# Kernel optimization log

Hardware: AMD Instinct MI355X
Metric: run time of the kernel (lower is better)

The kernel has to match this reference:

```python
import jax, jax.numpy as jnp
import numpy as np

H = 16  # n_heads

def _rmsnorm(x, g, eps=1e-6):
    return x * jax.lax.rsqrt(jnp.mean(x * x, axis=-1, keepdims=True) + eps) * g

def _rope_diag(L, hd, dtype):
    # Diagonal of the full [L, hd, hd] rotary matrix: cos(pos * theta_pair) at every dim.
    # (The torch einsum 'bhld,ldd->bhld' extracts this diagonal, so no pairwise rotation occurs.)
    pair = jnp.arange(hd) // 2
    theta = 10000.0 ** (-2.0 * pair / hd)
    return jnp.cos(jnp.arange(L)[:, None].astype(jnp.float32) * theta[None, :]).astype(dtype)


def setup_inputs() -> dict:
    key = jax.random.key(0)
    ks = jax.random.split(key, 8)
    B, L, E = 2, 2048, 2048
    F = 2 * E  # SwiGLU width
    s = 0.02
    return {
        "x": jax.random.normal(ks[0], (B, L, E), jnp.float32),
        "g": jnp.ones((E,), jnp.float32),
        "wq": jax.random.normal(ks[1], (E, E), jnp.float32) * s,
        "wk": jax.random.normal(ks[2], (E, E), jnp.float32) * s,
        "wv": jax.random.normal(ks[3], (E, E), jnp.float32) * s,
        "w1": jax.random.normal(ks[4], (E, F), jnp.float32) * s,
        "b1": jnp.zeros((F,), jnp.float32),
        "wg": jax.random.normal(ks[5], (F, F), jnp.float32) * s,
        "bg": jnp.zeros((F,), jnp.float32),
        "wl": jax.random.normal(ks[6], (F, F), jnp.float32) * s,
        "bl": jnp.zeros((F,), jnp.float32),
        "beta": jnp.ones((1,), jnp.float32),
        "w2": jax.random.normal(ks[7], (F, E), jnp.float32) * s,
        "b2": jnp.zeros((E,), jnp.float32),
    }


def reference(x, g, wq, wk, wv, w1, b1, wg, bg, wl, bl, beta, w2, b2):
    B, L, E = x.shape
    hd = E // H
    x_res = x
    h = _rmsnorm(x, g)
    # projections -> [B, H, L, hd]
    q = (h @ wq).reshape(B, L, H, hd).transpose(0, 2, 1, 3)
    k = (h @ wk).reshape(B, L, H, hd).transpose(0, 2, 1, 3)
    v = (h @ wv).reshape(B, L, H, hd).transpose(0, 2, 1, 3)
    D = _rope_diag(L, hd, x.dtype)  # [L, hd], diagonal of rotary matrix
    q = q * D
    k = k * D
    score = jnp.einsum('bhld,bhmd->bhlm', q, k)  # [B,H,L,L]
    # causal mask added BEFORE scaling (faithful to source)
    mask = jnp.triu(jnp.full((L, L), -jnp.inf, dtype=score.dtype), k=1)
    score = (score + mask) / jnp.sqrt(jnp.asarray(hd, score.dtype))
    attn = jax.nn.softmax(score, axis=-1)
    o = jnp.einsum('bhlm,bhmd->bhld', attn, v)
    o = o.transpose(0, 2, 1, 3).reshape(B, L, E)
    x = o + x_res
    x_res = x
    h = _rmsnorm(x, g)
    h = h @ w1 + b1  # [B, L, 2E]
    gate = h @ wg + bg
    lin = h @ wl + bl
    act = gate * jax.nn.sigmoid(beta * gate) * lin
    out = act @ w2 + b2
    return out + x_res
```

## Files before the change

### kernel.cpp

```cpp
#include <hip/hip_runtime.h>
#include <cstdint>
#include <math.h>


typedef _Float16 f16;
typedef _Float16 f16x8 __attribute__((ext_vector_type(8)));
typedef _Float16 f16x4 __attribute__((ext_vector_type(4)));
typedef float    f32x4 __attribute__((ext_vector_type(4)));

#define MFMA_16x16x32(a, b, c) __builtin_amdgcn_mfma_f32_16x16x32_f16(a, b, c, 0, 0, 0)

__device__ __forceinline__ void gload_lds16(const void* g, void* lds) {
  __builtin_amdgcn_global_load_lds(
      (__attribute__((address_space(1))) void*)(uintptr_t)g,
      (__attribute__((address_space(3))) void*)(unsigned)(uintptr_t)lds,
      16, 0, 0);
}

__global__ void convT_k(const float* __restrict__ W, f16* __restrict__ Wt,
                        int K, int N) {
  __shared__ float tile[32][33];
  const int n0 = blockIdx.x << 5, k0 = blockIdx.y << 5;
  const int t = threadIdx.x;
  const int r = t >> 3, c4 = (t & 7) << 2;
  const f32x4 v = *(const f32x4*)(W + (size_t)(k0 + r) * N + n0 + c4);
  tile[r][c4 + 0] = v[0]; tile[r][c4 + 1] = v[1];
  tile[r][c4 + 2] = v[2]; tile[r][c4 + 3] = v[3];
  __syncthreads();
  f16x4 o;
  o[0] = (f16)tile[c4 + 0][r]; o[1] = (f16)tile[c4 + 1][r];
  o[2] = (f16)tile[c4 + 2][r]; o[3] = (f16)tile[c4 + 3][r];
  *(f16x4*)(Wt + (size_t)(n0 + r) * K + k0 + c4) = o;
}

__global__ void rope_tab_k(float* __restrict__ Dt) {
  const int l = blockIdx.x, d = threadIdx.x;
  const float th = __expf(-0.0719557841f * (float)(d & ~1));
  Dt[(l << 7) + d] = cosf((float)l * th);
}

__global__ void rmsnorm_k(const float* __restrict__ X, const float* __restrict__ G,
                          f16* __restrict__ H) {
  __shared__ float red[4];
  const int row = blockIdx.x, t = threadIdx.x;
  const float* xp = X + ((size_t)row << 11) + (t << 3);
  const f32x4 v0 = *(const f32x4*)xp;
  const f32x4 v1 = *(const f32x4*)(xp + 4);
  float ss = v0[0]*v0[0] + v0[1]*v0[1] + v0[2]*v0[2] + v0[3]*v0[3]
           + v1[0]*v1[0] + v1[1]*v1[1] + v1[2]*v1[2] + v1[3]*v1[3];
#pragma unroll
  for (int m = 1; m < 64; m <<= 1) ss += __shfl_xor(ss, m);
  if ((t & 63) == 0) red[t >> 6] = ss;
  __syncthreads();
  const float tot = red[0] + red[1] + red[2] + red[3];
  const float rs = rsqrtf(tot * (1.f / 2048.f) + 1e-6f);
  const float* gp = G + (t << 3);
  const f32x4 g0 = *(const f32x4*)gp, g1 = *(const f32x4*)(gp + 4);
  f16x8 o;
  o[0] = (f16)(v0[0]*rs*g0[0]); o[1] = (f16)(v0[1]*rs*g0[1]);
  o[2] = (f16)(v0[2]*rs*g0[2]); o[3] = (f16)(v0[3]*rs*g0[3]);
  o[4] = (f16)(v1[0]*rs*g1[0]); o[5] = (f16)(v1[1]*rs*g1[1]);
  o[6] = (f16)(v1[2]*rs*g1[2]); o[7] = (f16)(v1[3]*rs*g1[3]);
  *(f16x8*)(H + ((size_t)row << 11) + (t << 3)) = o;
}

__global__ void vtrans_k(const f16* __restrict__ V, f16* __restrict__ Vt) {
  __shared__ f16 tile[32][36];
  const int l0 = blockIdx.x << 5, d0 = blockIdx.y << 5, bh = blockIdx.z;
  const int b = bh >> 4, h = bh & 15;
  const int t = threadIdx.x;
  const int r = t >> 3, c4 = (t & 7) << 2;
  const f16x4 v = *(const f16x4*)(V + (size_t)((b << 11) + l0 + r) * 2048 + (h << 7) + d0 + c4);
  tile[r][c4 + 0] = v[0]; tile[r][c4 + 1] = v[1];
  tile[r][c4 + 2] = v[2]; tile[r][c4 + 3] = v[3];
  __syncthreads();
  f16x4 o;
  o[0] = tile[c4 + 0][r]; o[1] = tile[c4 + 1][r];
  o[2] = tile[c4 + 2][r]; o[3] = tile[c4 + 3][r];
  *(f16x4*)(Vt + (size_t)((bh << 7) + d0 + r) * 2048 + l0 + c4) = o;
}

template <int EPI>
__launch_bounds__(256, 2)
__global__ void gemm_k(const f16* __restrict__ A, const f16* __restrict__ Bt,
                       void* __restrict__ Cout, int M, int N, int K,
                       const float* __restrict__ bias,
                       const float* __restrict__ auxf,
                       const f16* __restrict__ auxh,
                       const float* __restrict__ betap,
                       float scale) {
  __shared__ alignas(16) f16 As[128 * 64];
  __shared__ alignas(16) f16 Bs[128 * 64];
  const int t = threadIdx.x;
  const int lane = t & 63;
  const int w = t >> 6;
  const int wm = w >> 1, wn = w & 1;
  const int bm = blockIdx.y << 7;
  const int bn = blockIdx.x << 7;
  const int lh = lane & 15, lq = lane >> 4;

  f32x4 acc[4][4] = {};

  for (int k0 = 0; k0 < K; k0 += 64) {
    __syncthreads();
#pragma unroll
    for (int i = 0; i < 4; ++i) {
      const int idx = i * 256 + (w << 6) + lane;
      const int row = idx >> 3, c = idx & 7;
      const int cs = (c ^ (row & 7)) << 3;
      gload_lds16(A + (size_t)(bm + row) * K + k0 + cs,
                  &As[(i * 256 + (w << 6)) << 3]);
      gload_lds16(Bt + (size_t)(bn + row) * K + k0 + cs,
                  &Bs[(i * 256 + (w << 6)) << 3]);
    }
    asm volatile("s_waitcnt vmcnt(0)" ::: "memory");
    __syncthreads();
#pragma unroll
    for (int kk = 0; kk < 2; ++kk) {
      f16x8 af[4], bf[4];
#pragma unroll
      for (int mi = 0; mi < 4; ++mi) {
        const int r = (wm << 6) + (mi << 4) + lh;
        af[mi] = *(const f16x8*)&As[(r << 6) + ((((kk << 2) + lq) ^ (r & 7)) << 3)];
      }
#pragma unroll
      for (int ni = 0; ni < 4; ++ni) {
        const int r = (wn << 6) + (ni << 4) + lh;
        bf[ni] = *(const f16x8*)&Bs[(r << 6) + ((((kk << 2) + lq) ^ (r & 7)) << 3)];
      }
#pragma unroll
      for (int mi = 0; mi < 4; ++mi)
#pragma unroll
        for (int ni = 0; ni < 4; ++ni)
          acc[mi][ni] = MFMA_16x16x32(af[mi], bf[ni], acc[mi][ni]);
    }
  }

  const float be = (EPI == 3) ? betap[0] : 0.f;
#pragma unroll
  for (int mi = 0; mi < 4; ++mi) {
#pragma unroll
    for (int ni = 0; ni < 4; ++ni) {
#pragma unroll
      for (int r = 0; r < 4; ++r) {
        const int grow = bm + (wm << 6) + (mi << 4) + (lq << 2) + r;
        const int gcol = bn + (wn << 6) + (ni << 4) + lh;
        float v = acc[mi][ni][r];
        if (EPI >= 2) v += bias[gcol];
        const size_t off = (size_t)grow * N + gcol;
        if (EPI == 0) {
          v *= scale * auxf[((grow & 2047) << 7) + (gcol & 127)];
          ((f16*)Cout)[off] = (f16)v;
        } else if (EPI == 1 || EPI == 2) {
          ((f16*)Cout)[off] = (f16)v;
        } else if (EPI == 3) {
          ((f16*)Cout)[off] = (f16)(v / (1.f + __expf(-be * v)));
        } else if (EPI == 4) {
          ((f16*)Cout)[off] = (f16)(v * (float)auxh[off]);
        } else {
          ((float*)Cout)[off] = v + auxf[off];
        }
      }
    }
  }
}

__launch_bounds__(256, 2)
__global__ void attn_k(const f16* __restrict__ Q, const f16* __restrict__ Kb,
                       const f16* __restrict__ Vt, const float* __restrict__ Xres,
                       float* __restrict__ X2) {
  constexpr int L = 2048, E = 2048, HD = 128;
  __shared__ alignas(16) f16 Ks[64 * 128];
  __shared__ alignas(16) f16 Vs[128 * 64];
  __shared__ alignas(16) f16 Ps[4][32 * 72];

  const int t = threadIdx.x, lane = t & 63, w = t >> 6;
  const int q0 = blockIdx.x << 7;
  const int bh = blockIdx.y;
  const int b = bh >> 4, h = bh & 15;
  const int lh = lane & 15, lq = lane >> 4;
  const int wrow0 = q0 + (w << 5);

  f16x8 qf[2][4];
#pragma unroll
  for (int mi = 0; mi < 2; ++mi) {
    const f16* qrow = Q + (size_t)(b * L + wrow0 + (mi << 4) + lh) * E + h * HD;
#pragma unroll
    for (int kq = 0; kq < 4; ++kq)
      qf[mi][kq] = *(const f16x8*)(qrow + (kq << 5) + (lq << 3));
  }

  f32x4 oacc[2][8] = {};
  float mrun[2][4], lrun[2][4];
#pragma unroll
  for (int mi = 0; mi < 2; ++mi)
#pragma unroll
    for (int r = 0; r < 4; ++r) { mrun[mi][r] = -1e30f; lrun[mi][r] = 0.f; }

  const int nkv = q0 + 128;
  for (int kv0 = 0; kv0 < nkv; kv0 += 64) {
    __syncthreads();
#pragma unroll
    for (int i = 0; i < 4; ++i) {
      const int idx = i * 256 + (w << 6) + lane;
      {
        const int row = idx >> 4, c = idx & 15;
        gload_lds16(Kb + (size_t)(b * L + kv0 + row) * E + h * HD + ((c ^ (row & 7)) << 3),
                    &Ks[(i * 256 + (w << 6)) << 3]);
      }
      {
        const int row = idx >> 3, c = idx & 7;
        gload_lds16(Vt + ((size_t)bh * HD + row) * L + kv0 + ((c ^ (row & 7)) << 3),
                    &Vs[(i * 256 + (w << 6)) << 3]);
      }
    }
    asm volatile("s_waitcnt vmcnt(0)" ::: "memory");
    __syncthreads();

    if (kv0 <= wrow0 + 31) {
      f32x4 sacc[2][4] = {};
#pragma unroll
      for (int kq = 0; kq < 4; ++kq) {
        f16x8 kf[4];
#pragma unroll
        for (int ni = 0; ni < 4; ++ni) {
          const int r = (ni << 4) + lh;
          kf[ni] = *(const f16x8*)&Ks[(r << 7) + ((((kq << 2) + lq) ^ (r & 7)) << 3)];
        }
#pragma unroll
        for (int mi = 0; mi < 2; ++mi)
#pragma unroll
          for (int ni = 0; ni < 4; ++ni)
            sacc[mi][ni] = MFMA_16x16x32(qf[mi][kq], kf[ni], sacc[mi][ni]);
      }
      if (kv0 + 63 > wrow0) {
#pragma unroll
        for (int mi = 0; mi < 2; ++mi)
#pragma unroll
          for (int ni = 0; ni < 4; ++ni)
#pragma unroll
            for (int r = 0; r < 4; ++r) {
              const int qr = wrow0 + (mi << 4) + (lq << 2) + r;
              const int kv = kv0 + (ni << 4) + lh;
              if (kv > qr) sacc[mi][ni][r] = -1e30f;
            }
      }
      float scl[2][4], rsum[2][4];
#pragma unroll
      for (int mi = 0; mi < 2; ++mi)
#pragma unroll
        for (int r = 0; r < 4; ++r) {
          float v = fmaxf(fmaxf(sacc[mi][0][r], sacc[mi][1][r]),
                          fmaxf(sacc[mi][2][r], sacc[mi][3][r]));
          v = fmaxf(v, __shfl_xor(v, 1));
          v = fmaxf(v, __shfl_xor(v, 2));
          v = fmaxf(v, __shfl_xor(v, 4));
          v = fmaxf(v, __shfl_xor(v, 8));
          const float mnew = fmaxf(mrun[mi][r], v);
          scl[mi][r] = __expf(mrun[mi][r] - mnew);
          mrun[mi][r] = mnew;
          rsum[mi][r] = 0.f;
        }
#pragma unroll
      for (int mi = 0; mi < 2; ++mi)
#pragma unroll
        for (int ni = 0; ni < 4; ++ni)
#pragma unroll
          for (int r = 0; r < 4; ++r) {
            const float p = __expf(sacc[mi][ni][r] - mrun[mi][r]);
            rsum[mi][r] += p;
            Ps[w][((mi << 4) + (lq << 2) + r) * 72 + (ni << 4) + lh] = (f16)p;
          }
#pragma unroll
      for (int mi = 0; mi < 2; ++mi)
#pragma unroll
        for (int r = 0; r < 4; ++r) {
          float s = rsum[mi][r];
          s += __shfl_xor(s, 1);
          s += __shfl_xor(s, 2);
          s += __shfl_xor(s, 4);
          s += __shfl_xor(s, 8);
          lrun[mi][r] = lrun[mi][r] * scl[mi][r] + s;
        }
#pragma unroll
      for (int mi = 0; mi < 2; ++mi)
#pragma unroll
        for (int nd = 0; nd < 8; ++nd)
#pragma unroll
          for (int r = 0; r < 4; ++r) oacc[mi][nd][r] *= scl[mi][r];
#pragma unroll
      for (int kp = 0; kp < 2; ++kp) {
        f16x8 pf[2];
#pragma unroll
        for (int mi = 0; mi < 2; ++mi)
          pf[mi] = *(const f16x8*)&Ps[w][((mi << 4) + lh) * 72 + (kp << 5) + (lq << 3)];
#pragma unroll
        for (int nd = 0; nd < 8; ++nd) {
          const int r = (nd << 4) + lh;
          const f16x8 vf = *(const f16x8*)&Vs[(r << 6) + ((((kp << 2) + lq) ^ (r & 7)) << 3)];
#pragma unroll
          for (int mi = 0; mi < 2; ++mi)
            oacc[mi][nd] = MFMA_16x16x32(pf[mi], vf, oacc[mi][nd]);
        }
      }
    }
  }
#pragma unroll
  for (int mi = 0; mi < 2; ++mi)
#pragma unroll
    for (int nd = 0; nd < 8; ++nd)
#pragma unroll
      for (int r = 0; r < 4; ++r) {
        const int qr = wrow0 + (mi << 4) + (lq << 2) + r;
        const size_t off = (size_t)(b * L + qr) * E + h * HD + (nd << 4) + lh;
        X2[off] = oacc[mi][nd][r] / lrun[mi][r] + Xres[off];
      }
}

extern "C" void kernel_launch(void* const* d_in, const int* in_sizes, int n_in,
                              void* d_out, int out_size, void* d_ws, size_t ws_size,
                              hipStream_t stream) {
  const float* x    = (const float*)d_in[0];
  const float* g    = (const float*)d_in[1];
  const float* wq   = (const float*)d_in[2];
  const float* wk   = (const float*)d_in[3];
  const float* wv   = (const float*)d_in[4];
  const float* w1   = (const float*)d_in[5];
  const float* b1   = (const float*)d_in[6];
  const float* wgp  = (const float*)d_in[7];
  const float* bg   = (const float*)d_in[8];
  const float* wl   = (const float*)d_in[9];
  const float* bl   = (const float*)d_in[10];
  const float* beta = (const float*)d_in[11];
  const float* w2   = (const float*)d_in[12];
  const float* b2   = (const float*)d_in[13];

  constexpr size_t MB = 1ull << 20;
  char* ws = (char*)d_ws;
  f16*   wT   = (f16*)(ws + 0 * MB);
  float* Dt   = (float*)(ws + 32 * MB);
  f16*   hbuf = (f16*)(ws + 33 * MB);
  f16*   qbuf = (f16*)(ws + 49 * MB);
  f16*   kbuf = (f16*)(ws + 65 * MB);
  f16*   vbuf = (f16*)(ws + 81 * MB);
  f16*   vtb  = (f16*)(ws + 97 * MB);
  float* x2   = (float*)(ws + 113 * MB);
  f16*   a1   = (f16*)(ws + 49 * MB);
  f16*   sbuf = (f16*)(ws + 81 * MB);
  f16*   act  = (f16*)(ws + 145 * MB);
  (void)ws_size; (void)n_in; (void)in_sizes; (void)out_size;

  const dim3 blk(256);
  const float qscale = 0.08838834764831845f;

  rope_tab_k<<<2048, 128, 0, stream>>>(Dt);
  rmsnorm_k<<<4096, blk, 0, stream>>>(x, g, hbuf);

  convT_k<<<dim3(64, 64), blk, 0, stream>>>(wq, wT, 2048, 2048);
  gemm_k<0><<<dim3(16, 32), blk, 0, stream>>>(hbuf, wT, qbuf, 4096, 2048, 2048,
                                              nullptr, Dt, nullptr, nullptr, qscale);
  convT_k<<<dim3(64, 64), blk, 0, stream>>>(wk, wT, 2048, 2048);
  gemm_k<0><<<dim3(16, 32), blk, 0, stream>>>(hbuf, wT, kbuf, 4096, 2048, 2048,
                                              nullptr, Dt, nullptr, nullptr, 1.0f);
  convT_k<<<dim3(64, 64), blk, 0, stream>>>(wv, wT, 2048, 2048);
  gemm_k<1><<<dim3(16, 32), blk, 0, stream>>>(hbuf, wT, vbuf, 4096, 2048, 2048,
                                              nullptr, nullptr, nullptr, nullptr, 1.0f);
  vtrans_k<<<dim3(64, 4, 32), blk, 0, stream>>>(vbuf, vtb);

  attn_k<<<dim3(16, 32), blk, 0, stream>>>(qbuf, kbuf, vtb, x, x2);

  rmsnorm_k<<<4096, blk, 0, stream>>>(x2, g, hbuf);

  convT_k<<<dim3(128, 64), blk, 0, stream>>>(w1, wT, 2048, 4096);
  gemm_k<2><<<dim3(32, 32), blk, 0, stream>>>(hbuf, wT, a1, 4096, 4096, 2048,
                                              b1, nullptr, nullptr, nullptr, 1.0f);
  convT_k<<<dim3(128, 128), blk, 0, stream>>>(wgp, wT, 4096, 4096);
  gemm_k<3><<<dim3(32, 32), blk, 0, stream>>>(a1, wT, sbuf, 4096, 4096, 4096,
                                              bg, nullptr, nullptr, beta, 1.0f);
  convT_k<<<dim3(128, 128), blk, 0, stream>>>(wl, wT, 4096, 4096);
  gemm_k<4><<<dim3(32, 32), blk, 0, stream>>>(a1, wT, act, 4096, 4096, 4096,
                                              bl, nullptr, sbuf, nullptr, 1.0f);
  convT_k<<<dim3(64, 128), blk, 0, stream>>>(w2, wT, 4096, 2048);
  gemm_k<5><<<dim3(16, 32), blk, 0, stream>>>(act, wT, (float*)d_out, 4096, 2048, 4096,
                                              b2, x2, nullptr, nullptr, 1.0f);
}
```

Baseline: 765.5 us.

## Add pipelined 256x256 GEMM, fuse QKV projection, persistent causal attention scheduling

Introduces a 512-thread GEMM with 256x256 tiles and double-buffered LDS, plus interleaved prefetch and priority hints, for the QKV and FFN projections. The three Q/K/V projections become one GEMM over a concatenated transposed weight, with per-segment rope and scale applied in the epilogue. Attention becomes a persistent kernel that pulls work items from an atomic counter, taking the longest causal query blocks first to balance load. Costs include higher LDS and register use per block, and a memset plus atomic per block.

```diff
diff --git a/kernel.cpp b/kernel.cpp
--- a/kernel.cpp
+++ b/kernel.cpp
@@ -81,14 +81,145 @@
 }
 
 template <int EPI>
+__launch_bounds__(512, 2)
+__global__ void gemm256_k(const f16* __restrict__ A, const f16* __restrict__ Bt,
+                          void* __restrict__ Cout, int M, int N, int K,
+                          const float* __restrict__ bias,
+                          const float* __restrict__ auxf,
+                          const f16* __restrict__ auxh,
+                          const float* __restrict__ betap, float scale) {
+  __shared__ alignas(16) f16 lds[65536];
+  const int t = threadIdx.x, lane = t & 63, w = t >> 6;
+  const int wm = w >> 2, wn = w & 3;
+  const int bm = blockIdx.y << 8, bn = blockIdx.x << 8;
+  const int lh = lane & 15, lq = lane >> 4;
+  const int NT = K >> 6;
+  const int lrow = lane >> 3;
+  const int lco  = ((lane & 7) ^ lrow) << 3;
+
+  const f16* Agl = A  + (size_t)(bm + lrow) * K + lco;
+  const f16* Bgl = Bt + (size_t)(bn + lrow) * K + lco;
+  const int aw = w << 3;
+  const int bw = w << 4;
+
+  f32x4 acc[8][4] = {};
+  f16x8 bf[4][2];
+
+  auto stA = [&](int tile, int half) {
+    const int d = (tile & 1) << 15;
+    const int k0 = tile << 6;
+    const int r0 = aw + (half << 6);
+    gload_lds16(Agl + (size_t)r0 * K + k0, (void*)&lds[d + r0 * 64]);
+    gload_lds16(Agl + (size_t)(r0 + 128) * K + k0, (void*)&lds[d + (r0 + 128) * 64]);
+  };
+  auto stB = [&](int tile, int half) {
+    const int d = ((tile & 1) << 15) + 16384;
+    const int k0 = tile << 6;
+    const int r0 = bw + (half << 7);
+    gload_lds16(Bgl + (size_t)r0 * K + k0, (void*)&lds[d + r0 * 64]);
+    gload_lds16(Bgl + (size_t)(r0 + 8) * K + k0, (void*)&lds[d + (r0 + 8) * 64]);
+  };
+  auto ldA = [&](int d, int mi, int kk) {
+    const int r = (wm << 7) + (mi << 4) + lh;
+    return *(const f16x8*)&lds[(d << 15) + r * 64 + ((((kk << 2) + lq) ^ (lh & 7)) << 3)];
+  };
+  auto ldB = [&](int d, int ni, int kk) {
+    const int r = (wn << 6) + (ni << 4) + lh;
+    return *(const f16x8*)&lds[(d << 15) + 16384 + r * 64 + ((((kk << 2) + lq) ^ (lh & 7)) << 3)];
+  };
+
+  stB(0, 0); stB(0, 1); stA(0, 0); stA(0, 1);
+  stB(1, 0); stB(1, 1); stA(1, 0);
+  asm volatile("s_waitcnt vmcnt(6)" ::: "memory");
+  __builtin_amdgcn_s_barrier();
+
+  for (int tt = 0; tt < NT; tt += 2) {
+    const bool pf = (tt + 2 < NT);
+#pragma unroll
+    for (int hf = 0; hf < 2; ++hf) {
+#pragma unroll
+      for (int ph = 0; ph < 4; ++ph) {
+        f16x8 a0k0 = ldA(hf, 2 * ph, 0),     a0k1 = ldA(hf, 2 * ph, 1);
+        f16x8 a1k0 = ldA(hf, 2 * ph + 1, 0), a1k1 = ldA(hf, 2 * ph + 1, 1);
+        if (ph == 0) {
+#pragma unroll
+          for (int ni = 0; ni < 4; ++ni) {
+            bf[ni][0] = ldB(hf, ni, 0); bf[ni][1] = ldB(hf, ni, 1);
+          }
+        }
+        if (hf == 0) {
+          if (ph == 0) stA(tt + 1, 1);
+          else if (ph == 1) { if (pf) stB(tt + 2, 0); }
+          else if (ph == 2) { if (pf) stB(tt + 2, 1); }
+          else              { if (pf) stA(tt + 2, 0); }
+        } else {
+          if (ph == 0)      { if (pf) stA(tt + 2, 1); }
+          else if (ph == 1) { if (pf) stB(tt + 3, 0); }
+          else if (ph == 2) { if (pf) stB(tt + 3, 1); }
+          else              { if (pf) stA(tt + 3, 0); }
+        }
+        __builtin_amdgcn_s_barrier();
+        __builtin_amdgcn_sched_barrier(0);
+        __builtin_amdgcn_s_setprio(1);
+#pragma unroll
+        for (int ni = 0; ni < 4; ++ni) {
+          acc[2 * ph][ni]     = MFMA_16x16x32(a0k0, bf[ni][0], acc[2 * ph][ni]);
+          acc[2 * ph][ni]     = MFMA_16x16x32(a0k1, bf[ni][1], acc[2 * ph][ni]);
+          acc[2 * ph + 1][ni] = MFMA_16x16x32(a1k0, bf[ni][0], acc[2 * ph + 1][ni]);
+          acc[2 * ph + 1][ni] = MFMA_16x16x32(a1k1, bf[ni][1], acc[2 * ph + 1][ni]);
+        }
+        __builtin_amdgcn_s_setprio(0);
+        __builtin_amdgcn_sched_barrier(0);
+        if (ph == 3) {
+          if (hf == 0) {
+            if (pf) asm volatile("s_waitcnt vmcnt(6)" ::: "memory");
+            else    asm volatile("s_waitcnt vmcnt(0)" ::: "memory");
+          } else if (pf) {
+            asm volatile("s_waitcnt vmcnt(6)" ::: "memory");
+          }
+        }
+        __builtin_amdgcn_s_barrier();
+      }
+    }
+  }
+
+  const float be = (EPI == 3) ? betap[0] : 0.f;
+#pragma unroll
+  for (int mi = 0; mi < 8; ++mi) {
+#pragma unroll
+    for (int ni = 0; ni < 4; ++ni) {
+#pragma unroll
+      for (int r = 0; r < 4; ++r) {
+        const int grow = bm + (wm << 7) + (mi << 4) + (lq << 2) + r;
+        const int gcol = bn + (wn << 6) + (ni << 4) + lh;
+        float v = acc[mi][ni][r];
+        if (EPI >= 2 && EPI <= 4) v += bias[gcol];
+        if (EPI == 6) {
+          const int seg = gcol >> 11, c = gcol & 2047;
+          if (seg < 2) {
+            const float f = auxf[((grow & 2047) << 7) + (c & 127)];
+            v *= (seg == 0) ? scale * f : f;
+          }
+          ((f16*)Cout)[(size_t)seg * 8388608 + ((size_t)grow << 11) + c] = (f16)v;
+        } else if (EPI == 2) {
+          ((f16*)Cout)[(size_t)grow * N + gcol] = (f16)v;
+        } else if (EPI == 3) {
+          ((f16*)Cout)[(size_t)grow * N + gcol] = (f16)(v / (1.f + __expf(-be * v)));
+        } else if (EPI == 4) {
+          const size_t off = (size_t)grow * N + gcol;
+          ((f16*)Cout)[off] = (f16)(v * (float)auxh[off]);
+        }
+      }
+    }
+  }
+}
+
+template <int EPI>
 __launch_bounds__(256, 2)
 __global__ void gemm_k(const f16* __restrict__ A, const f16* __restrict__ Bt,
                        void* __restrict__ Cout, int M, int N, int K,
                        const float* __restrict__ bias,
-                       const float* __restrict__ auxf,
-                       const f16* __restrict__ auxh,
-                       const float* __restrict__ betap,
-                       float scale) {
+                       const float* __restrict__ auxf) {
   __shared__ alignas(16) f16 As[128 * 64];
   __shared__ alignas(16) f16 Bs[128 * 64];
   const int t = threadIdx.x;
@@ -117,7 +248,7 @@
     __syncthreads();
 #pragma unroll
     for (int kk = 0; kk < 2; ++kk) {
-      f16x8 af[4], bf[4];
+      f16x8 af[4], bfr[4];
 #pragma unroll
       for (int mi = 0; mi < 4; ++mi) {
         const int r = (wm << 6) + (mi << 4) + lh;
@@ -126,17 +257,16 @@
 #pragma unroll
       for (int ni = 0; ni < 4; ++ni) {
         const int r = (wn << 6) + (ni << 4) + lh;
-        bf[ni] = *(const f16x8*)&Bs[(r << 6) + ((((kk << 2) + lq) ^ (r & 7)) << 3)];
+        bfr[ni] = *(const f16x8*)&Bs[(r << 6) + ((((kk << 2) + lq) ^ (r & 7)) << 3)];
       }
 #pragma unroll
       for (int mi = 0; mi < 4; ++mi)
 #pragma unroll
         for (int ni = 0; ni < 4; ++ni)
-          acc[mi][ni] = MFMA_16x16x32(af[mi], bf[ni], acc[mi][ni]);
+          acc[mi][ni] = MFMA_16x16x32(af[mi], bfr[ni], acc[mi][ni]);
     }
   }
 
-  const float be = (EPI == 3) ? betap[0] : 0.f;
 #pragma unroll
   for (int mi = 0; mi < 4; ++mi) {
 #pragma unroll
@@ -145,21 +275,9 @@
       for (int r = 0; r < 4; ++r) {
         const int grow = bm + (wm << 6) + (mi << 4) + (lq << 2) + r;
         const int gcol = bn + (wn << 6) + (ni << 4) + lh;
-        float v = acc[mi][ni][r];
-        if (EPI >= 2) v += bias[gcol];
+        float v = acc[mi][ni][r] + bias[gcol];
         const size_t off = (size_t)grow * N + gcol;
-        if (EPI == 0) {
-          v *= scale * auxf[((grow & 2047) << 7) + (gcol & 127)];
-          ((f16*)Cout)[off] = (f16)v;
-        } else if (EPI == 1 || EPI == 2) {
-          ((f16*)Cout)[off] = (f16)v;
-        } else if (EPI == 3) {
-          ((f16*)Cout)[off] = (f16)(v / (1.f + __expf(-be * v)));
-        } else if (EPI == 4) {
-          ((f16*)Cout)[off] = (f16)(v * (float)auxh[off]);
-        } else {
-          ((float*)Cout)[off] = v + auxf[off];
-        }
+        ((float*)Cout)[off] = v + auxf[off];
       }
     }
   }
@@ -168,153 +286,161 @@
 __launch_bounds__(256, 2)
 __global__ void attn_k(const f16* __restrict__ Q, const f16* __restrict__ Kb,
                        const f16* __restrict__ Vt, const float* __restrict__ Xres,
-                       float* __restrict__ X2) {
+                       float* __restrict__ X2, int* __restrict__ qcnt) {
   constexpr int L = 2048, E = 2048, HD = 128;
   __shared__ alignas(16) f16 Ks[64 * 128];
   __shared__ alignas(16) f16 Vs[128 * 64];
   __shared__ alignas(16) f16 Ps[4][32 * 72];
+  __shared__ int s_item;
 
   const int t = threadIdx.x, lane = t & 63, w = t >> 6;
-  const int q0 = blockIdx.x << 7;
-  const int bh = blockIdx.y;
-  const int b = bh >> 4, h = bh & 15;
   const int lh = lane & 15, lq = lane >> 4;
-  const int wrow0 = q0 + (w << 5);
-
-  f16x8 qf[2][4];
-#pragma unroll
-  for (int mi = 0; mi < 2; ++mi) {
-    const f16* qrow = Q + (size_t)(b * L + wrow0 + (mi << 4) + lh) * E + h * HD;
-#pragma unroll
-    for (int kq = 0; kq < 4; ++kq)
-      qf[mi][kq] = *(const f16x8*)(qrow + (kq << 5) + (lq << 3));
+
+  for (;;) {
+    if (t == 0) s_item = atomicAdd(qcnt, 1);
+    __syncthreads();
+    const int item = s_item;
+    if (item >= 512) return;
+    const int bh = item & 31;
+    const int q0 = (15 - (item >> 5)) << 7;
+    const int b = bh >> 4, h = bh & 15;
+    const int wrow0 = q0 + (w << 5);
+
+    f16x8 qf[2][4];
+#pragma unroll
+    for (int mi = 0; mi < 2; ++mi) {
+      const f16* qrow = Q + (size_t)(b * L + wrow0 + (mi << 4) + lh) * E + h * HD;
+#pragma unroll
+      for (int kq = 0; kq < 4; ++kq)
+        qf[mi][kq] = *(const f16x8*)(qrow + (kq << 5) + (lq << 3));
+    }
+
+    f32x4 oacc[2][8] = {};
+    float mrun[2][4], lrun[2][4];
+#pragma unroll
+    for (int mi = 0; mi < 2; ++mi)
+#pragma unroll
+      for (int r = 0; r < 4; ++r) { mrun[mi][r] = -1e30f; lrun[mi][r] = 0.f; }
+
+    const int nkv = q0 + 128;
+    for (int kv0 = 0; kv0 < nkv; kv0 += 64) {
+      __syncthreads();
+#pragma unroll
+      for (int i = 0; i < 4; ++i) {
+        const int idx = i * 256 + (w << 6) + lane;
+        {
+          const int row = idx >> 4, c = idx & 15;
+          gload_lds16(Kb + (size_t)(b * L + kv0 + row) * E + h * HD + ((c ^ (row & 7)) << 3),
+                      &Ks[(i * 256 + (w << 6)) << 3]);
+        }
+        {
+          const int row = idx >> 3, c = idx & 7;
+          gload_lds16(Vt + ((size_t)bh * HD + row) * L + kv0 + ((c ^ (row & 7)) << 3),
+                      &Vs[(i * 256 + (w << 6)) << 3]);
+        }
+      }
+      asm volatile("s_waitcnt vmcnt(0)" ::: "memory");
+      __syncthreads();
+
+      if (kv0 <= wrow0 + 31) {
+        f32x4 sacc[2][4] = {};
+#pragma unroll
+        for (int kq = 0; kq < 4; ++kq) {
+          f16x8 kf[4];
+#pragma unroll
+          for (int ni = 0; ni < 4; ++ni) {
+            const int r = (ni << 4) + lh;
+            kf[ni] = *(const f16x8*)&Ks[(r << 7) + ((((kq << 2) + lq) ^ (r & 7)) << 3)];
+          }
+#pragma unroll
+          for (int mi = 0; mi < 2; ++mi)
+#pragma unroll
+            for (int ni = 0; ni < 4; ++ni)
+              sacc[mi][ni] = MFMA_16x16x32(qf[mi][kq], kf[ni], sacc[mi][ni]);
+        }
+        if (kv0 + 63 > wrow0) {
+#pragma unroll
+          for (int mi = 0; mi < 2; ++mi)
+#pragma unroll
+            for (int ni = 0; ni < 4; ++ni)
+#pragma unroll
+              for (int r = 0; r < 4; ++r) {
+                const int qr = wrow0 + (mi << 4) + (lq << 2) + r;
+                const int kv = kv0 + (ni << 4) + lh;
+                if (kv > qr) sacc[mi][ni][r] = -1e30f;
+              }
+        }
+        float scl[2][4], rsum[2][4];
+#pragma unroll
+        for (int mi = 0; mi < 2; ++mi)
+#pragma unroll
+          for (int r = 0; r < 4; ++r) {
+            float v = fmaxf(fmaxf(sacc[mi][0][r], sacc[mi][1][r]),
+                            fmaxf(sacc[mi][2][r], sacc[mi][3][r]));
+            v = fmaxf(v, __shfl_xor(v, 1));
+            v = fmaxf(v, __shfl_xor(v, 2));
+            v = fmaxf(v, __shfl_xor(v, 4));
+            v = fmaxf(v, __shfl_xor(v, 8));
+            const float mnew = fmaxf(mrun[mi][r], v);
+            scl[mi][r] = __expf(mrun[mi][r] - mnew);
+            mrun[mi][r] = mnew;
+            rsum[mi][r] = 0.f;
+          }
+#pragma unroll
+        for (int mi = 0; mi < 2; ++mi)
+#pragma unroll
+          for (int ni = 0; ni < 4; ++ni)
+#pragma unroll
+            for (int r = 0; r < 4; ++r) {
+              const float p = __expf(sacc[mi][ni][r] - mrun[mi][r]);
+              rsum[mi][r] += p;
+              Ps[w][((mi << 4) + (lq << 2) + r) * 72 + (ni << 4) + lh] = (f16)p;
+            }
+#pragma unroll
+        for (int mi = 0; mi < 2; ++mi)
+#pragma unroll
+          for (int r = 0; r < 4; ++r) {
+            float s = rsum[mi][r];
+            s += __shfl_xor(s, 1);
+            s += __shfl_xor(s, 2);
+            s += __shfl_xor(s, 4);
+            s += __shfl_xor(s, 8);
+            lrun[mi][r] = lrun[mi][r] * scl[mi][r] + s;
+          }
+#pragma unroll
+        for (int mi = 0; mi < 2; ++mi)
+#pragma unroll
+          for (int nd = 0; nd < 8; ++nd)
+#pragma unroll
+            for (int r = 0; r < 4; ++r) oacc[mi][nd][r] *= scl[mi][r];
+#pragma unroll
+        for (int kp = 0; kp < 2; ++kp) {
+          f16x8 pf[2];
+#pragma unroll
+          for (int mi = 0; mi < 2; ++mi)
+            pf[mi] = *(const f16x8*)&Ps[w][((mi << 4) + lh) * 72 + (kp << 5) + (lq << 3)];
+#pragma unroll
+          for (int nd = 0; nd < 8; ++nd) {
+            const int r = (nd << 4) + lh;
+            const f16x8 vf = *(const f16x8*)&Vs[(r << 6) + ((((kp << 2) + lq) ^ (r & 7)) << 3)];
+#pragma unroll
+            for (int mi = 0; mi < 2; ++mi)
+              oacc[mi][nd] = MFMA_16x16x32(pf[mi], vf, oacc[mi][nd]);
+          }
+        }
+      }
+    }
+#pragma unroll
+    for (int mi = 0; mi < 2; ++mi)
+#pragma unroll
+      for (int nd = 0; nd < 8; ++nd)
+#pragma unroll
+        for (int r = 0; r < 4; ++r) {
+          const int qr = wrow0 + (mi << 4) + (lq << 2) + r;
+          const size_t off = (size_t)(b * L + qr) * E + h * HD + (nd << 4) + lh;
+          X2[off] = oacc[mi][nd][r] / lrun[mi][r] + Xres[off];
+        }
   }
-
-  f32x4 oacc[2][8] = {};
-  float mrun[2][4], lrun[2][4];
-#pragma unroll
-  for (int mi = 0; mi < 2; ++mi)
-#pragma unroll
-    for (int r = 0; r < 4; ++r) { mrun[mi][r] = -1e30f; lrun[mi][r] = 0.f; }
-
-  const int nkv = q0 + 128;
-  for (int kv0 = 0; kv0 < nkv; kv0 += 64) {
-    __syncthreads();
-#pragma unroll
-    for (int i = 0; i < 4; ++i) {
-      const int idx = i * 256 + (w << 6) + lane;
-      {
-        const int row = idx >> 4, c = idx & 15;
-        gload_lds16(Kb + (size_t)(b * L + kv0 + row) * E + h * HD + ((c ^ (row & 7)) << 3),
-                    &Ks[(i * 256 + (w << 6)) << 3]);
-      }
-      {
-        const int row = idx >> 3, c = idx & 7;
-        gload_lds16(Vt + ((size_t)bh * HD + row) * L + kv0 + ((c ^ (row & 7)) << 3),
-                    &Vs[(i * 256 + (w << 6)) << 3]);
-      }
-    }
-    asm volatile("s_waitcnt vmcnt(0)" ::: "memory");
-    __syncthreads();
-
-    if (kv0 <= wrow0 + 31) {
-      f32x4 sacc[2][4] = {};
-#pragma unroll
-      for (int kq = 0; kq < 4; ++kq) {
-        f16x8 kf[4];
-#pragma unroll
-        for (int ni = 0; ni < 4; ++ni) {
-          const int r = (ni << 4) + lh;
-          kf[ni] = *(const f16x8*)&Ks[(r << 7) + ((((kq << 2) + lq) ^ (r & 7)) << 3)];
-        }
-#pragma unroll
-        for (int mi = 0; mi < 2; ++mi)
-#pragma unroll
-          for (int ni = 0; ni < 4; ++ni)
-            sacc[mi][ni] = MFMA_16x16x32(qf[mi][kq], kf[ni], sacc[mi][ni]);
-      }
-      if (kv0 + 63 > wrow0) {
-#pragma unroll
-        for (int mi = 0; mi < 2; ++mi)
-#pragma unroll
-          for (int ni = 0; ni < 4; ++ni)
-#pragma unroll
-            for (int r = 0; r < 4; ++r) {
-              const int qr = wrow0 + (mi << 4) + (lq << 2) + r;
-              const int kv = kv0 + (ni << 4) + lh;
-              if (kv > qr) sacc[mi][ni][r] = -1e30f;
-            }
-      }
-      float scl[2][4], rsum[2][4];
-#pragma unroll
-      for (int mi = 0; mi < 2; ++mi)
-#pragma unroll
-        for (int r = 0; r < 4; ++r) {
-          float v = fmaxf(fmaxf(sacc[mi][0][r], sacc[mi][1][r]),
-                          fmaxf(sacc[mi][2][r], sacc[mi][3][r]));
-          v = fmaxf(v, __shfl_xor(v, 1));
-          v = fmaxf(v, __shfl_xor(v, 2));
-          v = fmaxf(v, __shfl_xor(v, 4));
-          v = fmaxf(v, __shfl_xor(v, 8));
-          const float mnew = fmaxf(mrun[mi][r], v);
-          scl[mi][r] = __expf(mrun[mi][r] - mnew);
-          mrun[mi][r] = mnew;
-          rsum[mi][r] = 0.f;
-        }
-#pragma unroll
-      for (int mi = 0; mi < 2; ++mi)
-#pragma unroll
-        for (int ni = 0; ni < 4; ++ni)
-#pragma unroll
-          for (int r = 0; r < 4; ++r) {
-            const float p = __expf(sacc[mi][ni][r] - mrun[mi][r]);
-            rsum[mi][r] += p;
-            Ps[w][((mi << 4) + (lq << 2) + r) * 72 + (ni << 4) + lh] = (f16)p;
-          }
-#pragma unroll
-      for (int mi = 0; mi < 2; ++mi)
-#pragma unroll
-        for (int r = 0; r < 4; ++r) {
-          float s = rsum[mi][r];
-          s += __shfl_xor(s, 1);
-          s += __shfl_xor(s, 2);
-          s += __shfl_xor(s, 4);
-          s += __shfl_xor(s, 8);
-          lrun[mi][r] = lrun[mi][r] * scl[mi][r] + s;
-        }
-#pragma unroll
-      for (int mi = 0; mi < 2; ++mi)
-#pragma unroll
-        for (int nd = 0; nd < 8; ++nd)
-#pragma unroll
-          for (int r = 0; r < 4; ++r) oacc[mi][nd][r] *= scl[mi][r];
-#pragma unroll
-      for (int kp = 0; kp < 2; ++kp) {
-        f16x8 pf[2];
-#pragma unroll
-        for (int mi = 0; mi < 2; ++mi)
-          pf[mi] = *(const f16x8*)&Ps[w][((mi << 4) + lh) * 72 + (kp << 5) + (lq << 3)];
-#pragma unroll
-        for (int nd = 0; nd < 8; ++nd) {
-          const int r = (nd << 4) + lh;
-          const f16x8 vf = *(const f16x8*)&Vs[(r << 6) + ((((kp << 2) + lq) ^ (r & 7)) << 3)];
-#pragma unroll
-          for (int mi = 0; mi < 2; ++mi)
-            oacc[mi][nd] = MFMA_16x16x32(pf[mi], vf, oacc[mi][nd]);
-        }
-      }
-    }
-  }
-#pragma unroll
-  for (int mi = 0; mi < 2; ++mi)
-#pragma unroll
-    for (int nd = 0; nd < 8; ++nd)
-#pragma unroll
-      for (int r = 0; r < 4; ++r) {
-        const int qr = wrow0 + (mi << 4) + (lq << 2) + r;
-        const size_t off = (size_t)(b * L + qr) * E + h * HD + (nd << 4) + lh;
-        X2[off] = oacc[mi][nd][r] / lrun[mi][r] + Xres[off];
-      }
 }
 
 extern "C" void kernel_launch(void* const* d_in, const int* in_sizes, int n_in,
@@ -338,10 +464,10 @@
   constexpr size_t MB = 1ull << 20;
   char* ws = (char*)d_ws;
   f16*   wT   = (f16*)(ws + 0 * MB);
+  int*   qcnt = (int*)(ws + 31 * MB);
   float* Dt   = (float*)(ws + 32 * MB);
   f16*   hbuf = (f16*)(ws + 33 * MB);
-  f16*   qbuf = (f16*)(ws + 49 * MB);
-  f16*   kbuf = (f16*)(ws + 65 * MB);
+  f16*   qkv  = (f16*)(ws + 49 * MB);
   f16*   vbuf = (f16*)(ws + 81 * MB);
   f16*   vtb  = (f16*)(ws + 97 * MB);
   float* x2   = (float*)(ws + 113 * MB);
@@ -355,32 +481,29 @@
 
   rope_tab_k<<<2048, 128, 0, stream>>>(Dt);
   rmsnorm_k<<<4096, blk, 0, stream>>>(x, g, hbuf);
+  hipMemsetAsync(qcnt, 0, 4, stream);
 
   convT_k<<<dim3(64, 64), blk, 0, stream>>>(wq, wT, 2048, 2048);
-  gemm_k<0><<<dim3(16, 32), blk, 0, stream>>>(hbuf, wT, qbuf, 4096, 2048, 2048,
-                                              nullptr, Dt, nullptr, nullptr, qscale);
-  convT_k<<<dim3(64, 64), blk, 0, stream>>>(wk, wT, 2048, 2048);
-  gemm_k<0><<<dim3(16, 32), blk, 0, stream>>>(hbuf, wT, kbuf, 4096, 2048, 2048,
-                                              nullptr, Dt, nullptr, nullptr, 1.0f);
-  convT_k<<<dim3(64, 64), blk, 0, stream>>>(wv, wT, 2048, 2048);
-  gemm_k<1><<<dim3(16, 32), blk, 0, stream>>>(hbuf, wT, vbuf, 4096, 2048, 2048,
-                                              nullptr, nullptr, nullptr, nullptr, 1.0f);
+  convT_k<<<dim3(64, 64), blk, 0, stream>>>(wk, wT + (size_t)2048 * 2048, 2048, 2048);
+  convT_k<<<dim3(64, 64), blk, 0, stream>>>(wv, wT + (size_t)4096 * 2048, 2048, 2048);
+  gemm256_k<6><<<dim3(24, 16), 512, 0, stream>>>(hbuf, wT, qkv, 4096, 6144, 2048,
+                                                 nullptr, Dt, nullptr, nullptr, qscale);
   vtrans_k<<<dim3(64, 4, 32), blk, 0, stream>>>(vbuf, vtb);
 
-  attn_k<<<dim3(16, 32), blk, 0, stream>>>(qbuf, kbuf, vtb, x, x2);
+  attn_k<<<384, blk, 0, stream>>>(qkv, qkv + (size_t)8388608, vtb, x, x2, qcnt);
 
   rmsnorm_k<<<4096, blk, 0, stream>>>(x2, g, hbuf);
 
   convT_k<<<dim3(128, 64), blk, 0, stream>>>(w1, wT, 2048, 4096);
-  gemm_k<2><<<dim3(32, 32), blk, 0, stream>>>(hbuf, wT, a1, 4096, 4096, 2048,
-                                              b1, nullptr, nullptr, nullptr, 1.0f);
+  gemm256_k<2><<<dim3(16, 16), 512, 0, stream>>>(hbuf, wT, a1, 4096, 4096, 2048,
+                                                 b1, nullptr, nullptr, nullptr, 1.0f);
   convT_k<<<dim3(128, 128), blk, 0, stream>>>(wgp, wT, 4096, 4096);
-  gemm_k<3><<<dim3(32, 32), blk, 0, stream>>>(a1, wT, sbuf, 4096, 4096, 4096,
-                                              bg, nullptr, nullptr, beta, 1.0f);
+  gemm256_k<3><<<dim3(16, 16), 512, 0, stream>>>(a1, wT, sbuf, 4096, 4096, 4096,
+                                                 bg, nullptr, nullptr, beta, 1.0f);
   convT_k<<<dim3(128, 128), blk, 0, stream>>>(wl, wT, 4096, 4096);
-  gemm_k<4><<<dim3(32, 32), blk, 0, stream>>>(a1, wT, act, 4096, 4096, 4096,
-                                              bl, nullptr, sbuf, nullptr, 1.0f);
+  gemm256_k<4><<<dim3(16, 16), 512, 0, stream>>>(a1, wT, act, 4096, 4096, 4096,
+                                                 bl, nullptr, sbuf, nullptr, 1.0f);
   convT_k<<<dim3(64, 128), blk, 0, stream>>>(w2, wT, 4096, 2048);
   gemm_k<5><<<dim3(16, 32), blk, 0, stream>>>(act, wT, (float*)d_out, 4096, 2048, 4096,
-                                              b2, x2, nullptr, nullptr, 1.0f);
-}
+                                              b2, x2);
+}
```

Result: slower. 820.9 us (+7.2%).
